# Kernel tuning notes

Measured on AMD Instinct MI355X. Metric: run time of the kernel, lower is better.

The kernel has to match this reference:

```python
import jax, jax.numpy as jnp
import numpy as np
from jax import lax

D_MODEL = 1024
D_STATE = 16


def setup_inputs() -> dict:
    key = jax.random.key(0)
    ks = jax.random.split(key, 7)
    B, L = 4, 2048
    x = jax.random.normal(ks[0], (B, L, D_MODEL), dtype=jnp.float32)
    s = 1.0 / np.sqrt(D_MODEL)
    W_dt = jax.random.uniform(ks[1], (D_MODEL, D_MODEL), jnp.float32, -s, s)
    b_dt = jax.random.uniform(ks[2], (D_MODEL,), jnp.float32, -s, s)
    W_B = jax.random.uniform(ks[3], (D_STATE, D_MODEL), jnp.float32, -s, s)
    W_C = jax.random.uniform(ks[4], (D_STATE, D_MODEL), jnp.float32, -s, s)
    A = jax.random.normal(ks[5], (D_MODEL, D_STATE), dtype=jnp.float32)
    A_log = jnp.log(jnp.abs(A) + 1e-4)
    D = jnp.ones((D_MODEL,), dtype=jnp.float32)
    return {"x": x, "W_dt": W_dt, "b_dt": b_dt, "W_B": W_B, "W_C": W_C,
            "A_log": A_log, "D": D}


def reference(x, W_dt, b_dt, W_B, W_C, A_log, D):
    B, L, Dm = x.shape
    N = A_log.shape[1]
    dt = jax.nn.softplus(jnp.einsum('bld,ed->ble', x, W_dt) + b_dt)  # [B,L,D]
    Bp = jnp.einsum('bld,nd->bln', x, W_B)   # [B,L,N]
    Cp = jnp.einsum('bld,nd->bln', x, W_C)   # [B,L,N]
    A = -jnp.exp(A_log)                      # [D,N]
    dA = jnp.exp(dt[..., None] * A)          # [B,L,D,N]
    # fuse dB * x: dB[bldn] = dt*Bp; input term = dB * x
    dBx = dt[..., None] * Bp[:, :, None, :] * x[..., None]  # [B,L,D,N]

    def step(h, inp):
        dA_t, dBx_t, C_t, x_t = inp
        h = dA_t * h + dBx_t                              # [B,D,N]
        y = jnp.einsum('bdn,bn->bd', h, C_t) + D * x_t    # [B,D]
        return h, y

    h0 = jnp.zeros((B, Dm, N), dtype=x.dtype)
    xs = (jnp.swapaxes(dA, 0, 1), jnp.swapaxes(dBx, 0, 1),
          jnp.swapaxes(Cp, 0, 1), jnp.swapaxes(x, 0, 1))
    _, ys = lax.scan(step, h0, xs)           # ys: [L,B,D]
    return jnp.swapaxes(ys, 0, 1)            # [B,L,D]
```

## Files before the change

kernel.cpp:

```cpp
#include <hip/hip_runtime.h>
#include <hip/hip_bf16.h>
#include <math.h>

#define DM 1024
#define DS 16
#define BB 4
#define LL 2048
#define LC 32
#define NC (LL/LC)
#define MT 8192
#define NT64 16
#define NCT 17

typedef __attribute__((ext_vector_type(8))) short short8;
typedef __attribute__((ext_vector_type(4))) float floatx4;

__device__ __forceinline__ float softplus_fast(float v) {
  return fmaxf(v, 0.f) + __logf(1.f + __expf(-fabsf(v)));
}

__global__ __launch_bounds__(256) void convert_kernel(
    const float* __restrict__ X, const float* __restrict__ W_dt,
    const float* __restrict__ WB, const float* __restrict__ WC,
    __hip_bfloat16* __restrict__ Xb, __hip_bfloat16* __restrict__ Wx)
{
  const size_t i  = (size_t)blockIdx.x * 256 + threadIdx.x;
  const size_t NX = (size_t)MT * DM / 8;
  const size_t NW = (size_t)DM * DM / 8;
  const size_t NB = (size_t)DS * DM / 8;
  const float* src;
  __hip_bfloat16* dst;
  size_t u;
  if (i < NX)                { src = X;    dst = Xb;                        u = i; }
  else if (i < NX + NW)      { src = W_dt; dst = Wx;                        u = i - NX; }
  else if (i < NX + NW + NB) { src = WB;   dst = Wx + (size_t)1024 * DM;    u = i - NX - NW; }
  else if (i < NX + NW + 2 * NB) { src = WC; dst = Wx + (size_t)1040 * DM;  u = i - NX - NW - NB; }
  else {
    const size_t z = i - NX - NW - 2 * NB;
    const short8 zz = {0, 0, 0, 0, 0, 0, 0, 0};
    *(short8*)&Wx[(size_t)1056 * DM + z * 8] = zz;
    return;
  }
  const float4 a = *(const float4*)&src[u * 8];
  const float4 b = *(const float4*)&src[u * 8 + 4];
  union { short8 v; __hip_bfloat16 h[8]; } o;
  o.h[0] = __float2bfloat16(a.x); o.h[1] = __float2bfloat16(a.y);
  o.h[2] = __float2bfloat16(a.z); o.h[3] = __float2bfloat16(a.w);
  o.h[4] = __float2bfloat16(b.x); o.h[5] = __float2bfloat16(b.y);
  o.h[6] = __float2bfloat16(b.z); o.h[7] = __float2bfloat16(b.w);
  *(short8*)&dst[u * 8] = o.v;
}

__global__ __launch_bounds__(512, 4) void gemm_dt_mfma(
    const __hip_bfloat16* __restrict__ Xb, const __hip_bfloat16* __restrict__ Wx,
    const float* __restrict__ bias, __hip_bfloat16* __restrict__ DTb,
    float* __restrict__ BP, float* __restrict__ CP)
{
  __shared__ short As[2][256 * 64];
  __shared__ short Bs[2][64 * 64];
  const int tid  = threadIdx.x;
  const int lane = tid & 63;
  const int wid  = tid >> 6;
  const int wm   = wid >> 1, wn = wid & 1;

  const int bid  = blockIdx.x;
  const int tile = (bid & 7) * 68 + (bid >> 3);
  const int row0 = (tile / NCT) * 256;
  const int col0 = (tile % NCT) * 64;

  const floatx4 zero = {0.f, 0.f, 0.f, 0.f};
  floatx4 acc[4][2];
#pragma unroll
  for (int i = 0; i < 4; ++i)
#pragma unroll
    for (int j = 0; j < 2; ++j) acc[i][j] = zero;

  auto STAGE = [&](int buf, int t) {
    const int k0 = t * 64;
#pragma unroll
    for (int q = 0; q < 4; ++q) {
      const int fe = q * 512 + tid;
      const int r  = fe >> 3;
      const int kk = (fe & 7) ^ (r & 7);
      __builtin_amdgcn_global_load_lds(
          (const __attribute__((address_space(1))) void*)&Xb[(size_t)(row0 + r) * DM + k0 + kk * 8],
          (__attribute__((address_space(3))) void*)&As[buf][fe * 8], 16, 0, 0);
    }
    {
      const int fe = tid;
      const int r  = fe >> 3;
      const int kk = (fe & 7) ^ (r & 7);
      __builtin_amdgcn_global_load_lds(
          (const __attribute__((address_space(1))) void*)&Wx[(size_t)(col0 + r) * DM + k0 + kk * 8],
          (__attribute__((address_space(3))) void*)&Bs[buf][fe * 8], 16, 0, 0);
    }
  };

  const int fr = lane & 15;
  const int ks = lane >> 4;

  STAGE(0, 0);
  int cur = 0;
  for (int t = 0; t < NT64; ++t) {
    if (t + 1 < NT64) {
      STAGE(cur ^ 1, t + 1);
      asm volatile("s_waitcnt vmcnt(5)" ::: "memory");
    } else {
      asm volatile("s_waitcnt vmcnt(0)" ::: "memory");
    }
    __builtin_amdgcn_s_barrier();
    __builtin_amdgcn_sched_barrier(0);

    short8 af[4][2], bfr[2][2];
#pragma unroll
    for (int i = 0; i < 4; ++i) {
      const int ar = wm * 64 + i * 16 + fr;
#pragma unroll
      for (int s = 0; s < 2; ++s) {
        const int ch = (ks + 4 * s) ^ (ar & 7);
        af[i][s] = *(const short8*)&As[cur][ar * 64 + ch * 8];
      }
    }
#pragma unroll
    for (int j = 0; j < 2; ++j) {
      const int br = wn * 32 + j * 16 + fr;
#pragma unroll
      for (int s = 0; s < 2; ++s) {
        const int ch = (ks + 4 * s) ^ (br & 7);
        bfr[j][s] = *(const short8*)&Bs[cur][br * 64 + ch * 8];
      }
    }
    __builtin_amdgcn_s_setprio(1);
#pragma unroll
    for (int s = 0; s < 2; ++s)
#pragma unroll
      for (int i = 0; i < 4; ++i)
#pragma unroll
        for (int j = 0; j < 2; ++j)
          acc[i][j] = __builtin_amdgcn_mfma_f32_16x16x32_bf16(af[i][s], bfr[j][s], acc[i][j], 0, 0, 0);
    __builtin_amdgcn_s_setprio(0);
    __builtin_amdgcn_sched_barrier(0);

    if (t + 1 < NT64) {
      __builtin_amdgcn_s_barrier();
      cur ^= 1;
    }
  }

  const int cl = lane & 15;
  const int rg = lane >> 4;
  if (col0 < 1024) {
#pragma unroll
    for (int i = 0; i < 4; ++i) {
#pragma unroll
      for (int r = 0; r < 4; ++r) {
        const size_t row = (size_t)(row0 + wm * 64 + i * 16 + rg * 4 + r);
#pragma unroll
        for (int j = 0; j < 2; ++j) {
          const int col = col0 + wn * 32 + j * 16 + cl;
          const float v = acc[i][j][r] + bias[col];
          DTb[row * DM + col] = __float2bfloat16(softplus_fast(v));
        }
      }
    }
  } else if (wn == 0) {
#pragma unroll
    for (int i = 0; i < 4; ++i) {
#pragma unroll
      for (int r = 0; r < 4; ++r) {
        const size_t row = (size_t)(row0 + wm * 64 + i * 16 + rg * 4 + r);
        BP[row * DS + cl] = acc[i][0][r];
        CP[row * DS + cl] = acc[i][1][r];
      }
    }
  }
}

__global__ __launch_bounds__(256) void scan_partial_kernel(
    const __hip_bfloat16* __restrict__ DT, const __hip_bfloat16* __restrict__ X,
    const float* __restrict__ Bp, const float* __restrict__ A_log,
    float* __restrict__ SD, float* __restrict__ HP)
{
  __shared__ float sB[LC * DS];
  const int tid = threadIdx.x;
  const int d = blockIdx.x * 256 + tid;
  const int c = blockIdx.y;
  const int b = blockIdx.z;
  const int l0 = c * LC;

  if (tid < LC * DS / 4)
    ((float4*)sB)[tid] = ((const float4*)&Bp[((size_t)b * LL + l0) * DS])[tid];

  float A[DS], h[DS];
  float sdt = 0.f;
  const float4* arow = (const float4*)&A_log[(size_t)d * DS];
#pragma unroll
  for (int m = 0; m < 4; ++m) {
    const float4 a4 = arow[m];
    A[m*4+0] = -__expf(a4.x); A[m*4+1] = -__expf(a4.y);
    A[m*4+2] = -__expf(a4.z); A[m*4+3] = -__expf(a4.w);
  }
#pragma unroll
  for (int n = 0; n < DS; ++n) h[n] = 0.f;

  size_t idx = ((size_t)b * LL + l0) * DM + d;
  float dtb[4], xb[4];
#pragma unroll
  for (int u = 0; u < 4; ++u) {
    dtb[u] = __bfloat162float(DT[idx + (size_t)u * DM]);
    xb[u]  = __bfloat162float(X[idx + (size_t)u * DM]);
  }
  __syncthreads();

  for (int l = 0; l < LC; l += 4) {
    float dtn[4], xn[4];
    if (l + 4 < LC) {
#pragma unroll
      for (int u = 0; u < 4; ++u) {
        dtn[u] = __bfloat162float(DT[idx + (size_t)(u + 4) * DM]);
        xn[u]  = __bfloat162float(X[idx + (size_t)(u + 4) * DM]);
      }
    }
#pragma unroll
    for (int u = 0; u < 4; ++u) {
      const float dtv = dtb[u], xv = xb[u];
      const float dx = dtv * xv;
      sdt += dtv;
      const float4 b0 = ((const float4*)sB)[(l+u)*4+0];
      const float4 b1 = ((const float4*)sB)[(l+u)*4+1];
      const float4 b2 = ((const float4*)sB)[(l+u)*4+2];
      const float4 b3 = ((const float4*)sB)[(l+u)*4+3];
      const float bb[DS] = {b0.x,b0.y,b0.z,b0.w, b1.x,b1.y,b1.z,b1.w,
                            b2.x,b2.y,b2.z,b2.w, b3.x,b3.y,b3.z,b3.w};
#pragma unroll
      for (int n = 0; n < DS; ++n) {
        const float dA = __expf(dtv * A[n]);
        h[n] = fmaf(dA, h[n], dx * bb[n]);
      }
    }
    idx += (size_t)4 * DM;
#pragma unroll
    for (int u = 0; u < 4; ++u) { dtb[u] = dtn[u]; xb[u] = xn[u]; }
  }
  SD[((size_t)b * NC + c) * DM + d] = sdt;
  const size_t o = (((size_t)b * NC + c) * DM + d) * DS;
  float4* hp = (float4*)&HP[o];
#pragma unroll
  for (int m = 0; m < 4; ++m)
    hp[m] = make_float4(h[m*4+0], h[m*4+1], h[m*4+2], h[m*4+3]);
}

__global__ __launch_bounds__(256) void combine_kernel(
    const float* __restrict__ SD, const float* __restrict__ A_log,
    float* HP)
{
  const int idx = blockIdx.x * 256 + threadIdx.x;
  const int b  = idx >> 14;
  const int dn = idx & 16383;
  const int d  = dn >> 4;
  const float A = -__expf(A_log[dn]);
  float h = 0.f;
#pragma unroll 4
  for (int c = 0; c < NC; ++c) {
    const size_t o = (((size_t)b * NC + c) << 14) + dn;
    const float p  = __expf(SD[((size_t)b * NC + c) * DM + d] * A);
    const float hp = HP[o];
    HP[o] = h;
    h = fmaf(p, h, hp);
  }
}

__global__ __launch_bounds__(256) void scan_final_kernel(
    const __hip_bfloat16* __restrict__ DT, const __hip_bfloat16* __restrict__ X,
    const float* __restrict__ Bp, const float* __restrict__ Cp,
    const float* __restrict__ A_log, const float* __restrict__ Dvec,
    const float* __restrict__ Hin, float* __restrict__ Y)
{
  __shared__ float sB[LC * DS], sC[LC * DS];
  const int tid = threadIdx.x;
  const int d = blockIdx.x * 256 + tid;
  const int c = blockIdx.y;
  const int b = blockIdx.z;
  const int l0 = c * LC;

  if (tid < 128)       ((float4*)sB)[tid] = ((const float4*)&Bp[((size_t)b * LL + l0) * DS])[tid];
  else                 ((float4*)sC)[tid - 128] = ((const float4*)&Cp[((size_t)b * LL + l0) * DS])[tid - 128];

  float A[DS], h[DS];
  const float4* arow = (const float4*)&A_log[(size_t)d * DS];
  const size_t o = (((size_t)b * NC + c) * DM + d) * DS;
  const float4* hin = (const float4*)&Hin[o];
#pragma unroll
  for (int m = 0; m < 4; ++m) {
    const float4 a4 = arow[m];
    A[m*4+0] = -__expf(a4.x); A[m*4+1] = -__expf(a4.y);
    A[m*4+2] = -__expf(a4.z); A[m*4+3] = -__expf(a4.w);
    const float4 h4 = hin[m];
    h[m*4+0] = h4.x; h[m*4+1] = h4.y; h[m*4+2] = h4.z; h[m*4+3] = h4.w;
  }
  const float Dd = Dvec[d];
  size_t idx = ((size_t)b * LL + l0) * DM + d;

  float dtb[4], xb[4];
#pragma unroll
  for (int u = 0; u < 4; ++u) {
    dtb[u] = __bfloat162float(DT[idx + (size_t)u * DM]);
    xb[u]  = __bfloat162float(X[idx + (size_t)u * DM]);
  }
  __syncthreads();

  for (int l = 0; l < LC; l += 4) {
    float dtn[4], xn[4];
    if (l + 4 < LC) {
#pragma unroll
      for (int u = 0; u < 4; ++u) {
        dtn[u] = __bfloat162float(DT[idx + (size_t)(u + 4) * DM]);
        xn[u]  = __bfloat162float(X[idx + (size_t)(u + 4) * DM]);
      }
    }
#pragma unroll
    for (int u = 0; u < 4; ++u) {
      const float dtv = dtb[u], xv = xb[u];
      const float dx = dtv * xv;
      const float4 b0 = ((const float4*)sB)[(l+u)*4+0];
      const float4 b1 = ((const float4*)sB)[(l+u)*4+1];
      const float4 b2 = ((const float4*)sB)[(l+u)*4+2];
      const float4 b3 = ((const float4*)sB)[(l+u)*4+3];
      const float bb[DS] = {b0.x,b0.y,b0.z,b0.w, b1.x,b1.y,b1.z,b1.w,
                            b2.x,b2.y,b2.z,b2.w, b3.x,b3.y,b3.z,b3.w};
      const float4 c0 = ((const float4*)sC)[(l+u)*4+0];
      const float4 c1 = ((const float4*)sC)[(l+u)*4+1];
      const float4 c2 = ((const float4*)sC)[(l+u)*4+2];
      const float4 c3 = ((const float4*)sC)[(l+u)*4+3];
      const float cc[DS] = {c0.x,c0.y,c0.z,c0.w, c1.x,c1.y,c1.z,c1.w,
                            c2.x,c2.y,c2.z,c2.w, c3.x,c3.y,c3.z,c3.w};
      float y = 0.f;
#pragma unroll
      for (int n = 0; n < DS; ++n) {
        const float dA = __expf(dtv * A[n]);
        h[n] = fmaf(dA, h[n], dx * bb[n]);
        y = fmaf(h[n], cc[n], y);
      }
      Y[idx + (size_t)u * DM] = fmaf(Dd, xv, y);
    }
    idx += (size_t)4 * DM;
#pragma unroll
    for (int u = 0; u < 4; ++u) { dtb[u] = dtn[u]; xb[u] = xn[u]; }
  }
}

extern "C" void kernel_launch(void* const* d_in, const int* in_sizes, int n_in,
                              void* d_out, int out_size, void* d_ws, size_t ws_size,
                              hipStream_t stream)
{
  const float* x     = (const float*)d_in[0];
  const float* W_dt  = (const float*)d_in[1];
  const float* b_dt  = (const float*)d_in[2];
  const float* W_B   = (const float*)d_in[3];
  const float* W_C   = (const float*)d_in[4];
  const float* A_log = (const float*)d_in[5];
  const float* Dv    = (const float*)d_in[6];
  float* Y  = (float*)d_out;
  float* ws = (float*)d_ws;

  __hip_bfloat16* DTb = (__hip_bfloat16*)ws;
  float* BP = ws + (size_t)MT * DM / 2;
  float* CP = BP + (size_t)MT * DS;
  __hip_bfloat16* Xb = (__hip_bfloat16*)(CP + (size_t)MT * DS);
  __hip_bfloat16* Wx = (__hip_bfloat16*)(CP + (size_t)MT * DS + (size_t)MT * DM / 2);
  float* SD = CP + (size_t)MT * DS + (size_t)MT * DM / 2 + (size_t)1088 * DM / 2;
  float* HP = SD + (size_t)BB * NC * DM;

  convert_kernel<<<4640, 256, 0, stream>>>(x, W_dt, W_B, W_C, Xb, Wx);
  gemm_dt_mfma<<<544, 512, 0, stream>>>(Xb, Wx, b_dt, DTb, BP, CP);
  scan_partial_kernel<<<dim3(DM / 256, NC, BB), 256, 0, stream>>>(DTb, Xb, BP, A_log, SD, HP);
  combine_kernel<<<(BB * DM * DS) / 256, 256, 0, stream>>>(SD, A_log, HP);
  scan_final_kernel<<<dim3(DM / 256, NC, BB), 256, 0, stream>>>(DTb, Xb, BP, CP, A_log, Dv, HP, Y);
}
```

Baseline: 117.5 us.

## Retile dt GEMM to square 128x128 tiles and double scan chunk length

The projection GEMM moves from 256x64 tiles with 512 threads to 128x128 tiles with 256 threads. Each wave now computes a 64x64 sub-tile, which raises MFMA work per LDS fragment load, and the padded weight matrix grows to 1152 rows. The scan chunk length doubles from 32 to 64, halving the number of chunks and the partial-state traffic through the combine step, at the cost of fewer parallel blocks and a longer serial loop in each scan kernel. The padded B/C columns now take a full 128-wide tile, so more of the extra GEMM work is wasted on zero padding.

```diff
diff --git a/kernel.cpp b/kernel.cpp
--- a/kernel.cpp
+++ b/kernel.cpp
@@ -6,11 +6,12 @@
 #define DS 16
 #define BB 4
 #define LL 2048
-#define LC 32
+#define LC 64
 #define NC (LL/LC)
 #define MT 8192
 #define NT64 16
-#define NCT 17
+#define NCT2 9
+#define WROWS 1152
 
 typedef __attribute__((ext_vector_type(8))) short short8;
 typedef __attribute__((ext_vector_type(4))) float floatx4;
@@ -51,45 +52,40 @@
   *(short8*)&dst[u * 8] = o.v;
 }
 
-__global__ __launch_bounds__(512, 4) void gemm_dt_mfma(
+__global__ __launch_bounds__(256) void gemm_dt_mfma(
     const __hip_bfloat16* __restrict__ Xb, const __hip_bfloat16* __restrict__ Wx,
     const float* __restrict__ bias, __hip_bfloat16* __restrict__ DTb,
     float* __restrict__ BP, float* __restrict__ CP)
 {
-  __shared__ short As[2][256 * 64];
-  __shared__ short Bs[2][64 * 64];
+  __shared__ short As[2][128 * 64];
+  __shared__ short Bs[2][128 * 64];
   const int tid  = threadIdx.x;
   const int lane = tid & 63;
   const int wid  = tid >> 6;
   const int wm   = wid >> 1, wn = wid & 1;
 
   const int bid  = blockIdx.x;
-  const int tile = (bid & 7) * 68 + (bid >> 3);
-  const int row0 = (tile / NCT) * 256;
-  const int col0 = (tile % NCT) * 64;
+  const int tile = (bid & 7) * 72 + (bid >> 3);
+  const int row0 = (tile / NCT2) * 128;
+  const int col0 = (tile % NCT2) * 128;
 
   const floatx4 zero = {0.f, 0.f, 0.f, 0.f};
-  floatx4 acc[4][2];
+  floatx4 acc[4][4];
 #pragma unroll
   for (int i = 0; i < 4; ++i)
 #pragma unroll
-    for (int j = 0; j < 2; ++j) acc[i][j] = zero;
+    for (int j = 0; j < 4; ++j) acc[i][j] = zero;
 
   auto STAGE = [&](int buf, int t) {
     const int k0 = t * 64;
 #pragma unroll
     for (int q = 0; q < 4; ++q) {
-      const int fe = q * 512 + tid;
+      const int fe = q * 256 + tid;
       const int r  = fe >> 3;
       const int kk = (fe & 7) ^ (r & 7);
       __builtin_amdgcn_global_load_lds(
           (const __attribute__((address_space(1))) void*)&Xb[(size_t)(row0 + r) * DM + k0 + kk * 8],
           (__attribute__((address_space(3))) void*)&As[buf][fe * 8], 16, 0, 0);
-    }
-    {
-      const int fe = tid;
-      const int r  = fe >> 3;
-      const int kk = (fe & 7) ^ (r & 7);
       __builtin_amdgcn_global_load_lds(
           (const __attribute__((address_space(1))) void*)&Wx[(size_t)(col0 + r) * DM + k0 + kk * 8],
           (__attribute__((address_space(3))) void*)&Bs[buf][fe * 8], 16, 0, 0);
@@ -104,41 +100,36 @@
   for (int t = 0; t < NT64; ++t) {
     if (t + 1 < NT64) {
       STAGE(cur ^ 1, t + 1);
-      asm volatile("s_waitcnt vmcnt(5)" ::: "memory");
+      asm volatile("s_waitcnt vmcnt(8)" ::: "memory");
     } else {
       asm volatile("s_waitcnt vmcnt(0)" ::: "memory");
     }
     __builtin_amdgcn_s_barrier();
     __builtin_amdgcn_sched_barrier(0);
 
-    short8 af[4][2], bfr[2][2];
-#pragma unroll
-    for (int i = 0; i < 4; ++i) {
-      const int ar = wm * 64 + i * 16 + fr;
-#pragma unroll
-      for (int s = 0; s < 2; ++s) {
+#pragma unroll
+    for (int s = 0; s < 2; ++s) {
+      short8 af[4], bfr[4];
+#pragma unroll
+      for (int i = 0; i < 4; ++i) {
+        const int ar = wm * 64 + i * 16 + fr;
         const int ch = (ks + 4 * s) ^ (ar & 7);
-        af[i][s] = *(const short8*)&As[cur][ar * 64 + ch * 8];
-      }
-    }
-#pragma unroll
-    for (int j = 0; j < 2; ++j) {
-      const int br = wn * 32 + j * 16 + fr;
-#pragma unroll
-      for (int s = 0; s < 2; ++s) {
+        af[i] = *(const short8*)&As[cur][ar * 64 + ch * 8];
+      }
+#pragma unroll
+      for (int j = 0; j < 4; ++j) {
+        const int br = wn * 64 + j * 16 + fr;
         const int ch = (ks + 4 * s) ^ (br & 7);
-        bfr[j][s] = *(const short8*)&Bs[cur][br * 64 + ch * 8];
-      }
-    }
-    __builtin_amdgcn_s_setprio(1);
-#pragma unroll
-    for (int s = 0; s < 2; ++s)
+        bfr[j] = *(const short8*)&Bs[cur][br * 64 + ch * 8];
+      }
+      __builtin_amdgcn_s_setprio(1);
 #pragma unroll
       for (int i = 0; i < 4; ++i)
 #pragma unroll
-        for (int j = 0; j < 2; ++j)
-          acc[i][j] = __builtin_amdgcn_mfma_f32_16x16x32_bf16(af[i][s], bfr[j][s], acc[i][j], 0, 0, 0);
-    __builtin_amdgcn_s_setprio(0);
+        for (int j = 0; j < 4; ++j)
+          acc[i][j] = __builtin_amdgcn_mfma_f32_16x16x32_bf16(af[i], bfr[j], acc[i][j], 0, 0, 0);
+      __builtin_amdgcn_s_setprio(0);
+    }
     __builtin_amdgcn_sched_barrier(0);
 
     if (t + 1 < NT64) {
@@ -156,8 +147,8 @@
       for (int r = 0; r < 4; ++r) {
         const size_t row = (size_t)(row0 + wm * 64 + i * 16 + rg * 4 + r);
 #pragma unroll
-        for (int j = 0; j < 2; ++j) {
-          const int col = col0 + wn * 32 + j * 16 + cl;
+        for (int j = 0; j < 4; ++j) {
+          const int col = col0 + wn * 64 + j * 16 + cl;
           const float v = acc[i][j][r] + bias[col];
           DTb[row * DM + col] = __float2bfloat16(softplus_fast(v));
         }
@@ -188,8 +179,7 @@
   const int b = blockIdx.z;
   const int l0 = c * LC;
 
-  if (tid < LC * DS / 4)
-    ((float4*)sB)[tid] = ((const float4*)&Bp[((size_t)b * LL + l0) * DS])[tid];
+  ((float4*)sB)[tid] = ((const float4*)&Bp[((size_t)b * LL + l0) * DS])[tid];
 
   float A[DS], h[DS];
   float sdt = 0.f;
@@ -283,8 +273,8 @@
   const int b = blockIdx.z;
   const int l0 = c * LC;
 
-  if (tid < 128)       ((float4*)sB)[tid] = ((const float4*)&Bp[((size_t)b * LL + l0) * DS])[tid];
-  else                 ((float4*)sC)[tid - 128] = ((const float4*)&Cp[((size_t)b * LL + l0) * DS])[tid - 128];
+  ((float4*)sB)[tid] = ((const float4*)&Bp[((size_t)b * LL + l0) * DS])[tid];
+  ((float4*)sC)[tid] = ((const float4*)&Cp[((size_t)b * LL + l0) * DS])[tid];
 
   float A[DS], h[DS];
   const float4* arow = (const float4*)&A_log[(size_t)d * DS];
@@ -368,11 +358,11 @@
   float* CP = BP + (size_t)MT * DS;
   __hip_bfloat16* Xb = (__hip_bfloat16*)(CP + (size_t)MT * DS);
   __hip_bfloat16* Wx = (__hip_bfloat16*)(CP + (size_t)MT * DS + (size_t)MT * DM / 2);
-  float* SD = CP + (size_t)MT * DS + (size_t)MT * DM / 2 + (size_t)1088 * DM / 2;
+  float* SD = CP + (size_t)MT * DS + (size_t)MT * DM / 2 + (size_t)WROWS * DM / 2;
   float* HP = SD + (size_t)BB * NC * DM;
 
-  convert_kernel<<<4640, 256, 0, stream>>>(x, W_dt, W_B, W_C, Xb, Wx);
-  gemm_dt_mfma<<<544, 512, 0, stream>>>(Xb, Wx, b_dt, DTb, BP, CP);
+  convert_kernel<<<4672, 256, 0, stream>>>(x, W_dt, W_B, W_C, Xb, Wx);
+  gemm_dt_mfma<<<576, 256, 0, stream>>>(Xb, Wx, b_dt, DTb, BP, CP);
   scan_partial_kernel<<<dim3(DM / 256, NC, BB), 256, 0, stream>>>(DTb, Xb, BP, A_log, SD, HP);
   combine_kernel<<<(BB * DM * DS) / 256, 256, 0, stream>>>(SD, A_log, HP);
   scan_final_kernel<<<dim3(DM / 256, NC, BB), 256, 0, stream>>>(DTb, Xb, BP, CP, A_log, Dv, HP, Y);
```

Result: slower. 125.6 us (+6.9%).
